# Optimization experiments

Measured on AMD Instinct MI355X. Metric: run time of the kernel, lower is better.

Reference implementation:

```python
import jax, jax.numpy as jnp
import numpy as np

B, L, D, H = 2, 2048, 1024, 16
DH = D // H
TAU = 0.1


def setup_inputs() -> dict:
    key = jax.random.key(0)
    ks = jax.random.split(key, 12)
    s = 0.02
    return {
        "q_x": jax.random.normal(ks[0], (B, L, D), jnp.float32),
        "k_x": jax.random.normal(ks[1], (B, L, D), jnp.float32),
        "v_x": jax.random.normal(ks[2], (B, L, D), jnp.float32),
        "ec": jax.random.normal(ks[3], (B, L, D), jnp.float32),
        "Wq": jax.random.normal(ks[4], (D, D), jnp.float32) * s,
        "bq": jnp.zeros((D,), jnp.float32),
        "Wk": jax.random.normal(ks[5], (D, D), jnp.float32) * s,
        "bk": jnp.zeros((D,), jnp.float32),
        "Wv": jax.random.normal(ks[6], (D, D), jnp.float32) * s,
        "bv": jnp.zeros((D,), jnp.float32),
        "Wo": jax.random.normal(ks[7], (D, D), jnp.float32) * s,
        "bo": jnp.zeros((D,), jnp.float32),
    }


def reference(q_x, k_x, v_x, ec, Wq, bq, Wk, bk, Wv, bv, Wo, bo):
    # torch nn.Linear: y = x @ W.T + b
    Q = (q_x @ Wq.T + bq).reshape(B, L, H, DH).transpose(0, 2, 1, 3)   # [B,H,L,Dh]
    K = (k_x @ Wk.T + bk).reshape(B, -1, H, DH).transpose(0, 2, 1, 3)  # [B,H,S,Dh]
    V = (v_x @ Wv.T + bv).reshape(B, -1, H, DH).transpose(0, 2, 1, 3)  # [B,H,S,Dh]
    scores = jnp.einsum("bhld,bhsd->bhls", Q, K) / jnp.sqrt(jnp.float32(DH))
    w = jnp.nan_to_num(jax.nn.softmax(scores, axis=-1), nan=0.0)       # [B,H,L,S]
    # frequency gate per key position: sigmoid((mean|ec| - tau) * 10)
    gate = jax.nn.sigmoid((jnp.abs(ec).mean(-1) - TAU) * 10.0)          # [B,S]
    w = w * gate[:, None, None, :]
    out = jnp.einsum("bhls,bhsd->bhld", w, V)                           # [B,H,L,Dh]
    out = out.transpose(0, 2, 1, 3).reshape(B, L, D)
    return out @ Wo.T + bo
```

## Files before the change

kernel.cpp:

```cpp
#include <hip/hip_runtime.h>

typedef unsigned short u16;
typedef unsigned int u32;
typedef unsigned long long u64;
typedef __attribute__((ext_vector_type(8))) short bf16x8;
typedef __attribute__((ext_vector_type(4))) float f32x4;
typedef __attribute__((ext_vector_type(2))) unsigned int u32x2;
typedef __attribute__((ext_vector_type(4))) unsigned int u32x4;

#define B_ 2
#define L_ 2048
#define D_ 1024
#define H_ 16
#define M_ 4096

__device__ __forceinline__ u16 f2bf(float f) {
  u32 x = __builtin_bit_cast(u32, f);
  return (u16)((x + 0x7fffu + ((x >> 16) & 1u)) >> 16);
}
__device__ __forceinline__ u32 cvtpk(float lo, float hi) {
  u32 r;
  asm("v_cvt_pk_bf16_f32 %0, %1, %2" : "=v"(r) : "v"(lo), "v"(hi));
  return r;
}

__device__ __forceinline__ void lane_regroup(u32& a, u32& b) {
#if __has_builtin(__builtin_amdgcn_permlane32_swap) && \
    __has_builtin(__builtin_amdgcn_permlane16_swap)
  u32x2 r = __builtin_amdgcn_permlane32_swap(a, b, false, false);
  u32x2 t = __builtin_amdgcn_permlane16_swap(r.x, r.y, false, false);
  a = t.x;
  b = t.y;
#else
  asm("v_permlane32_swap_b32 %0, %1\n\t"
      "v_permlane16_swap_b32 %0, %1"
      : "+v"(a), "+v"(b));
#endif
}

__device__ __forceinline__ void gl2lds16(void* lds, const void* g) {
  __builtin_amdgcn_global_load_lds(
      (const __attribute__((address_space(1))) u32*)g,
      (__attribute__((address_space(3))) u32*)lds, 16, 0, 0);
}

__device__ __forceinline__ void wait_vm8() {
  asm volatile("s_waitcnt vmcnt(8)" ::: "memory");
}
__device__ __forceinline__ void wait_vm6() {
  asm volatile("s_waitcnt vmcnt(6)" ::: "memory");
}
__device__ __forceinline__ void wait_vm4() {
  asm volatile("s_waitcnt vmcnt(4)" ::: "memory");
}
__device__ __forceinline__ void wait_vm0() {
  asm volatile("s_waitcnt vmcnt(0)" ::: "memory");
}
__device__ __forceinline__ void bar() {
  asm volatile("" ::: "memory");
  __builtin_amdgcn_s_barrier();
  asm volatile("" ::: "memory");
}

__global__ void cvt_all(const float* __restrict__ q, const float* __restrict__ k,
                        const float* __restrict__ v, const float* __restrict__ wq,
                        const float* __restrict__ wk, const float* __restrict__ wv,
                        const float* __restrict__ wo, const float* __restrict__ ec,
                        u16* __restrict__ Xq, u16* __restrict__ Xk, u16* __restrict__ Xv,
                        u16* __restrict__ Wqb, u16* __restrict__ Wkb,
                        u16* __restrict__ Wvb, u16* __restrict__ Wob,
                        float* __restrict__ gate) {
  if (blockIdx.x >= 16384) {
    int row = (blockIdx.x - 16384) * 4 + (threadIdx.x >> 6);
    int lane = threadIdx.x & 63;
    const float4* p = (const float4*)(ec + (size_t)row * 1024);
    float s = 0.f;
#pragma unroll
    for (int i = 0; i < 4; i++) {
      float4 vv = p[i * 64 + lane];
      s += fabsf(vv.x) + fabsf(vv.y) + fabsf(vv.z) + fabsf(vv.w);
    }
#pragma unroll
    for (int m = 1; m < 64; m <<= 1) s += __shfl_xor(s, m);
    if (lane == 0) {
      float mean = s * (1.0f / 1024.0f);
      gate[row] = 1.0f / (1.0f + __expf(-(mean - 0.1f) * 10.0f));
    }
    return;
  }
  int i = blockIdx.x * 256 + threadIdx.x;
  const float* s;
  u16* d;
  int off;
  if (i < 3145728) {
    int t = i >> 20;
    off = i & 1048575;
    s = t == 0 ? q : t == 1 ? k : v;
    d = t == 0 ? Xq : t == 1 ? Xk : Xv;
  } else {
    int j = i - 3145728;
    int t = j >> 18;
    off = j & 262143;
    s = t == 0 ? wq : t == 1 ? wk : t == 2 ? wv : wo;
    d = t == 0 ? Wqb : t == 1 ? Wkb : t == 2 ? Wvb : Wob;
  }
  float4 vv = ((const float4*)s)[off];
  ((u64*)d)[off] = (u64)cvtpk(vv.x, vv.y) | ((u64)cvtpk(vv.z, vv.w) << 32);
}

__global__ __launch_bounds__(256, 3) void gemm_qkv(
    const u16* __restrict__ Xq, const u16* __restrict__ Xk, const u16* __restrict__ Xv,
    const u16* __restrict__ Wq, const u16* __restrict__ Wk, const u16* __restrict__ Wv,
    const float* __restrict__ bq, const float* __restrict__ bk,
    const float* __restrict__ bv, const float* __restrict__ gate,
    u16* __restrict__ Qo, u16* __restrict__ Ko, u16* __restrict__ Vt) {
  __shared__ char smem[49152];
  const int which = blockIdx.x >> 9;
  const u16* A = which == 0 ? Xq : which == 1 ? Xk : Xv;
  const u16* Bw = which == 0 ? Wq : which == 1 ? Wk : Wv;
  const float* bias = which == 0 ? bq : which == 1 ? bk : bv;
  const int bi = blockIdx.x & 511;
  const int tid = threadIdx.x;
  const int tm = bi >> 3;
  const int tn = bi & 7;
  const int w = tid >> 6, lane = tid & 63;
  const int c = lane & 15, g = lane >> 4;
  const int wr = (w >> 1) << 5;
  const int wc = (w & 1) << 6;
  const int srow = tid >> 3, sch = tid & 7;

  f32x4 acc[2][4] = {};

  auto stage = [&](int buf, int t) {
    char* As = smem + buf * 24576;
    char* Bs = As + 8192;
#pragma unroll
    for (int i = 0; i < 2; i++) {
      int row = i * 32 + srow;
      int chs = (sch ^ (row & 7)) << 3;
      gl2lds16(As + i * 4096 + w * 1024, A + (size_t)(tm * 64 + row) * 1024 + t * 64 + chs);
    }
#pragma unroll
    for (int i = 0; i < 4; i++) {
      int row = i * 32 + srow;
      int chs = (sch ^ (row & 7)) << 3;
      gl2lds16(Bs + i * 4096 + w * 1024, Bw + (size_t)(tn * 128 + row) * 1024 + t * 64 + chs);
    }
  };

  stage(0, 0);
  for (int t = 0; t < 16; t++) {
    int cur = t & 1;
    if (t < 15) {
      stage(cur ^ 1, t + 1);
      wait_vm6();
    } else {
      wait_vm0();
    }
    bar();
    const char* As = smem + cur * 24576;
    const char* Bs = As + 8192;
#pragma unroll
    for (int kd = 0; kd < 2; kd++) {
      bf16x8 af[2], bfr[4];
#pragma unroll
      for (int fi = 0; fi < 2; fi++) {
        int ra = wr + fi * 16 + c;
        af[fi] = *(const bf16x8*)(As + ra * 128 + ((((kd << 2) | g) ^ (ra & 7)) << 4));
      }
#pragma unroll
      for (int fj = 0; fj < 4; fj++) {
        int rb = wc + fj * 16 + c;
        bfr[fj] = *(const bf16x8*)(Bs + rb * 128 + ((((kd << 2) | g) ^ (rb & 7)) << 4));
      }
#pragma unroll
      for (int fi = 0; fi < 2; fi++)
#pragma unroll
        for (int fj = 0; fj < 4; fj++)
          acc[fi][fj] = __builtin_amdgcn_mfma_f32_16x16x32_bf16(af[fi], bfr[fj],
                                                                acc[fi][fj], 0, 0, 0);
    }
    bar();
  }

  if (which == 2) {
    u16* T = (u16*)smem;
    __syncthreads();
#pragma unroll
    for (int fi = 0; fi < 2; fi++) {
      int lr0 = wr + fi * 16 + g * 4;
      float4 gg = *(const float4*)(gate + tm * 64 + lr0);
#pragma unroll
      for (int fj = 0; fj < 4; fj++) {
        int lc = wc + fj * 16 + c;
        float bv2 = bias[tn * 128 + lc];
        T[lc * 72 + lr0 + 0] = f2bf((acc[fi][fj][0] + bv2) * gg.x);
        T[lc * 72 + lr0 + 1] = f2bf((acc[fi][fj][1] + bv2) * gg.y);
        T[lc * 72 + lr0 + 2] = f2bf((acc[fi][fj][2] + bv2) * gg.z);
        T[lc * 72 + lr0 + 3] = f2bf((acc[fi][fj][3] + bv2) * gg.w);
      }
    }
    __syncthreads();
    const int lc = tid >> 1, hf = tid & 1;
    const int vtrow = (tm >> 5) * 1024 + tn * 128 + lc;
    const int s0 = (tm & 31) * 64 + hf * 32;
    const u16* src = T + lc * 72 + hf * 32;
    u16* dst = Vt + (size_t)vtrow * 2048 + s0;
#pragma unroll
    for (int j = 0; j < 4; j++)
      *(bf16x8*)(dst + j * 8) = *(const bf16x8*)(src + j * 8);
  } else {
    u16* Cout = which == 0 ? Qo : Ko;
    const float oscl = which == 0 ? 0.18033688011112042f : 1.0f;
    const int rowb = tm * 64 + wr + g * 4;
    const int colb = tn * 128 + wc + c;
#pragma unroll
    for (int fj = 0; fj < 4; fj++) {
      int col = colb + fj * 16;
      float bv2 = bias[col];
#pragma unroll
      for (int fi = 0; fi < 2; fi++) {
        int r0 = rowb + fi * 16;
#pragma unroll
        for (int r = 0; r < 4; r++)
          Cout[(size_t)(r0 + r) * 1024 + col] = f2bf((acc[fi][fj][r] + bv2) * oscl);
      }
    }
  }
}

__global__ __launch_bounds__(256, 2) void gemm_o(const u16* __restrict__ A,
                                                 const u16* __restrict__ Bw,
                                                 const float* __restrict__ bias,
                                                 float* __restrict__ Cout) {
  __shared__ char smem[49152];
  const int tid = threadIdx.x;
  const int tm = blockIdx.x >> 3;
  const int tn = blockIdx.x & 7;
  const int w = tid >> 6, lane = tid & 63;
  const int c = lane & 15, g = lane >> 4;
  const int wr = (w >> 1) << 5;
  const int wc = (w & 1) << 6;
  const int srow = tid >> 3, sch = tid & 7;

  f32x4 acc[2][4] = {};

  auto stage = [&](int buf, int t) {
    char* As = smem + buf * 24576;
    char* Bs = As + 8192;
#pragma unroll
    for (int i = 0; i < 2; i++) {
      int row = i * 32 + srow;
      int chs = (sch ^ (row & 7)) << 3;
      gl2lds16(As + i * 4096 + w * 1024, A + (size_t)(tm * 64 + row) * 1024 + t * 64 + chs);
    }
#pragma unroll
    for (int i = 0; i < 4; i++) {
      int row = i * 32 + srow;
      int chs = (sch ^ (row & 7)) << 3;
      gl2lds16(Bs + i * 4096 + w * 1024, Bw + (size_t)(tn * 128 + row) * 1024 + t * 64 + chs);
    }
  };

  stage(0, 0);
  for (int t = 0; t < 16; t++) {
    int cur = t & 1;
    if (t < 15) {
      stage(cur ^ 1, t + 1);
      wait_vm6();
    } else {
      wait_vm0();
    }
    bar();
    const char* As = smem + cur * 24576;
    const char* Bs = As + 8192;
#pragma unroll
    for (int kd = 0; kd < 2; kd++) {
      bf16x8 af[2], bfr[4];
#pragma unroll
      for (int fi = 0; fi < 2; fi++) {
        int ra = wr + fi * 16 + c;
        af[fi] = *(const bf16x8*)(As + ra * 128 + ((((kd << 2) | g) ^ (ra & 7)) << 4));
      }
#pragma unroll
      for (int fj = 0; fj < 4; fj++) {
        int rb = wc + fj * 16 + c;
        bfr[fj] = *(const bf16x8*)(Bs + rb * 128 + ((((kd << 2) | g) ^ (rb & 7)) << 4));
      }
#pragma unroll
      for (int fi = 0; fi < 2; fi++)
#pragma unroll
        for (int fj = 0; fj < 4; fj++)
          acc[fi][fj] = __builtin_amdgcn_mfma_f32_16x16x32_bf16(af[fi], bfr[fj],
                                                                acc[fi][fj], 0, 0, 0);
    }
    bar();
  }

  const int rowb = tm * 64 + wr + g * 4;
  const int colb = tn * 128 + wc + c;
#pragma unroll
  for (int fj = 0; fj < 4; fj++) {
    int col = colb + fj * 16;
    float bv2 = bias[col];
#pragma unroll
    for (int fi = 0; fi < 2; fi++) {
      int r0 = rowb + fi * 16;
#pragma unroll
      for (int r = 0; r < 4; r++)
        Cout[(size_t)(r0 + r) * 1024 + col] = acc[fi][fj][r] + bv2;
    }
  }
}

__global__ __launch_bounds__(256, 3) void attn_kernel(const u16* __restrict__ Qb,
                                                      const u16* __restrict__ Kb,
                                                      const u16* __restrict__ Vt,
                                                      u16* __restrict__ Ob) {
  __shared__ char asmem[49152];
  const int bi = blockIdx.x;
  const int bh = (bi & 7) | ((bi >> 7) << 3);
  const int qt = (bi >> 3) & 15;
  const int b = bh >> 4, h = bh & 15;
  const int tid = threadIdx.x, w = tid >> 6, lane = tid & 63;
  const int c = lane & 15, g = lane >> 4;
  const int qrow0 = b * L_ + qt * 128 + w * 32;

  bf16x8 qf[2][2];
#pragma unroll
  for (int fj = 0; fj < 2; fj++)
#pragma unroll
    for (int kd = 0; kd < 2; kd++)
      qf[fj][kd] = *(const bf16x8*)(Qb + (size_t)(qrow0 + fj * 16 + c) * D_ + h * 64 +
                                    kd * 32 + g * 8);

  const u32x4 onew = {0x3F803F80u, 0x3F803F80u, 0x3F803F80u, 0x3F803F80u};
  const bf16x8 one8 = __builtin_bit_cast(bf16x8, onew);

  f32x4 oacc[4][2] = {};
  f32x4 oaccD[2] = {};

  const int srow = tid >> 3, sch = tid & 7;
  const int vrow = tid >> 4, vch = tid & 15;

  auto stageK = [&](int buf, int kv) {
    char* KsB = asmem + buf * 16384;
    int sbase = kv * 128;
#pragma unroll
    for (int i = 0; i < 4; i++) {
      int kr = i * 32 + srow;
      gl2lds16(KsB + i * 4096 + w * 1024,
               Kb + (size_t)(b * L_ + sbase + kr) * D_ + h * 64 + ((sch ^ (kr & 7)) << 3));
    }
  };
  auto stageV = [&](int kv) {
    char* VsB = asmem + 32768;
    int sbase = kv * 128;
#pragma unroll
    for (int i = 0; i < 4; i++) {
      int vr = i * 16 + vrow;
      gl2lds16(VsB + i * 4096 + w * 1024,
               Vt + (size_t)(bh * 64 + vr) * 2048 + sbase + ((vch ^ (vr & 15)) << 3));
    }
  };

  stageK(0, 0);
  stageV(0);
  int buf = 0;
  for (int kv = 0; kv < 16; kv++) {
    if (kv < 15) {
      stageK(buf ^ 1, kv + 1);
      wait_vm8();
    } else {
      wait_vm4();
    }
    bar();
    const char* Ks = asmem + buf * 16384;
    const char* Vs = asmem + 32768;

    f32x4 st0[8] = {}, st1[8] = {};
    __builtin_amdgcn_s_setprio(1);
#pragma unroll
    for (int kd = 0; kd < 2; kd++) {
#pragma unroll
      for (int fi = 0; fi < 8; fi++) {
        int row = fi * 16 + c;
        bf16x8 kf = *(const bf16x8*)(Ks + row * 128 + ((((kd << 2) | g) ^ (c & 7)) << 4));
        st0[fi] = __builtin_amdgcn_mfma_f32_16x16x32_bf16(kf, qf[0][kd], st0[fi], 0, 0, 0);
        st1[fi] = __builtin_amdgcn_mfma_f32_16x16x32_bf16(kf, qf[1][kd], st1[fi], 0, 0, 0);
      }
    }
    __builtin_amdgcn_s_setprio(0);

    u32 pkA0[8], pkB0[8], pkA1[8], pkB1[8];
#pragma unroll
    for (int fi = 0; fi < 8; fi++) {
      pkA0[fi] = cvtpk(__builtin_amdgcn_exp2f(st0[fi][0]), __builtin_amdgcn_exp2f(st0[fi][1]));
      pkB0[fi] = cvtpk(__builtin_amdgcn_exp2f(st0[fi][2]), __builtin_amdgcn_exp2f(st0[fi][3]));
    }
#pragma unroll
    for (int fi = 0; fi < 8; fi++) {
      pkA1[fi] = cvtpk(__builtin_amdgcn_exp2f(st1[fi][0]), __builtin_amdgcn_exp2f(st1[fi][1]));
      pkB1[fi] = cvtpk(__builtin_amdgcn_exp2f(st1[fi][2]), __builtin_amdgcn_exp2f(st1[fi][3]));
    }

    if (kv < 15)
      wait_vm4();
    else
      wait_vm0();

    __builtin_amdgcn_s_setprio(1);
#pragma unroll
    for (int ks = 0; ks < 4; ks++) {
      u32 a0 = pkA0[2 * ks], b0 = pkA0[2 * ks + 1];
      lane_regroup(a0, b0);
      u32 a1 = pkB0[2 * ks], b1 = pkB0[2 * ks + 1];
      lane_regroup(a1, b1);
      u32x4 pw0 = {a0, a1, b0, b1};
      bf16x8 pf0 = __builtin_bit_cast(bf16x8, pw0);
      u32 e0 = pkA1[2 * ks], f0 = pkA1[2 * ks + 1];
      lane_regroup(e0, f0);
      u32 e1 = pkB1[2 * ks], f1 = pkB1[2 * ks + 1];
      lane_regroup(e1, f1);
      u32x4 pw1 = {e0, e1, f0, f1};
      bf16x8 pf1 = __builtin_bit_cast(bf16x8, pw1);
      oaccD[0] = __builtin_amdgcn_mfma_f32_16x16x32_bf16(one8, pf0, oaccD[0], 0, 0, 0);
      oaccD[1] = __builtin_amdgcn_mfma_f32_16x16x32_bf16(one8, pf1, oaccD[1], 0, 0, 0);
#pragma unroll
      for (int fd = 0; fd < 4; fd++) {
        int vr2 = fd * 16 + c;
        bf16x8 vf = *(const bf16x8*)(Vs + vr2 * 256 + ((((ks << 2) | g) ^ (vr2 & 15)) << 4));
        oacc[fd][0] = __builtin_amdgcn_mfma_f32_16x16x32_bf16(vf, pf0, oacc[fd][0], 0, 0, 0);
        oacc[fd][1] = __builtin_amdgcn_mfma_f32_16x16x32_bf16(vf, pf1, oacc[fd][1], 0, 0, 0);
      }
    }
    __builtin_amdgcn_s_setprio(0);
    bar();
    if (kv < 15) stageV(kv + 1);
    buf ^= 1;
  }

#pragma unroll
  for (int fj = 0; fj < 2; fj++) {
    float inv = 1.0f / oaccD[fj][0];
    size_t orow = (size_t)(qrow0 + fj * 16 + c) * D_ + h * 64;
#pragma unroll
    for (int fd = 0; fd < 4; fd++) {
      u64 pk = (u64)cvtpk(oacc[fd][fj][0] * inv, oacc[fd][fj][1] * inv) |
               ((u64)cvtpk(oacc[fd][fj][2] * inv, oacc[fd][fj][3] * inv) << 32);
      *(u64*)(Ob + orow + fd * 16 + g * 4) = pk;
    }
  }
}

extern "C" void kernel_launch(void* const* d_in, const int* in_sizes, int n_in,
                              void* d_out, int out_size, void* d_ws, size_t ws_size,
                              hipStream_t stream) {
  const float* q_x = (const float*)d_in[0];
  const float* k_x = (const float*)d_in[1];
  const float* v_x = (const float*)d_in[2];
  const float* ec = (const float*)d_in[3];
  const float* Wq = (const float*)d_in[4];
  const float* bq = (const float*)d_in[5];
  const float* Wk = (const float*)d_in[6];
  const float* bk = (const float*)d_in[7];
  const float* Wv = (const float*)d_in[8];
  const float* bv = (const float*)d_in[9];
  const float* Wo = (const float*)d_in[10];
  const float* bo = (const float*)d_in[11];

  char* ws = (char*)d_ws;
  const size_t MB = 1024 * 1024;
  u16* Wqb = (u16*)(ws + 0 * MB);
  u16* Wkb = (u16*)(ws + 2 * MB);
  u16* Wvb = (u16*)(ws + 4 * MB);
  u16* Wob = (u16*)(ws + 6 * MB);
  float* gatep = (float*)(ws + 8 * MB);
  u16* Xq = (u16*)(ws + 9 * MB);
  u16* Xk = (u16*)(ws + 17 * MB);
  u16* Xv = (u16*)(ws + 25 * MB);
  u16* Qb = (u16*)(ws + 33 * MB);
  u16* Kb = (u16*)(ws + 41 * MB);
  u16* Vtb = (u16*)(ws + 49 * MB);
  u16* Ab = Xk;

  cvt_all<<<17408, 256, 0, stream>>>(q_x, k_x, v_x, Wq, Wk, Wv, Wo, ec, Xq, Xk, Xv,
                                     Wqb, Wkb, Wvb, Wob, gatep);
  gemm_qkv<<<1536, 256, 0, stream>>>(Xq, Xk, Xv, Wqb, Wkb, Wvb, bq, bk, bv, gatep, Qb,
                                     Kb, Vtb);
  attn_kernel<<<512, 256, 0, stream>>>(Qb, Kb, Vtb, Ab);
  gemm_o<<<512, 256, 0, stream>>>(Ab, Wob, bo, (float*)d_out);
}
```

Baseline: 115.0 us.

## Fuse fp32-to-bf16 activation conversion into QKV GEMM A-tile loading

Removes the separate conversion pass for the three fp32 activation tensors. The QKV GEMM now loads fp32 A tiles into registers, converts them to bf16 and writes them into swizzled LDS, with the next tile's load issued before the MFMA loop. This drops a 24MB write and reread of bf16 copies but doubles the GEMM's A-side global traffic and replaces async global-to-LDS loads with register staging that raises register pressure.

```diff
diff --git a/kernel.cpp b/kernel.cpp
--- a/kernel.cpp
+++ b/kernel.cpp
@@ -56,22 +56,22 @@
 __device__ __forceinline__ void wait_vm0() {
   asm volatile("s_waitcnt vmcnt(0)" ::: "memory");
 }
+__device__ __forceinline__ void wait_lgkm0() {
+  asm volatile("s_waitcnt lgkmcnt(0)" ::: "memory");
+}
 __device__ __forceinline__ void bar() {
   asm volatile("" ::: "memory");
   __builtin_amdgcn_s_barrier();
   asm volatile("" ::: "memory");
 }
 
-__global__ void cvt_all(const float* __restrict__ q, const float* __restrict__ k,
-                        const float* __restrict__ v, const float* __restrict__ wq,
-                        const float* __restrict__ wk, const float* __restrict__ wv,
-                        const float* __restrict__ wo, const float* __restrict__ ec,
-                        u16* __restrict__ Xq, u16* __restrict__ Xk, u16* __restrict__ Xv,
-                        u16* __restrict__ Wqb, u16* __restrict__ Wkb,
-                        u16* __restrict__ Wvb, u16* __restrict__ Wob,
-                        float* __restrict__ gate) {
-  if (blockIdx.x >= 16384) {
-    int row = (blockIdx.x - 16384) * 4 + (threadIdx.x >> 6);
+__global__ void cvt_all(const float* __restrict__ wq, const float* __restrict__ wk,
+                        const float* __restrict__ wv, const float* __restrict__ wo,
+                        const float* __restrict__ ec, u16* __restrict__ Wqb,
+                        u16* __restrict__ Wkb, u16* __restrict__ Wvb,
+                        u16* __restrict__ Wob, float* __restrict__ gate) {
+  if (blockIdx.x >= 4096) {
+    int row = (blockIdx.x - 4096) * 4 + (threadIdx.x >> 6);
     int lane = threadIdx.x & 63;
     const float4* p = (const float4*)(ec + (size_t)row * 1024);
     float s = 0.f;
@@ -89,34 +89,24 @@
     return;
   }
   int i = blockIdx.x * 256 + threadIdx.x;
-  const float* s;
-  u16* d;
-  int off;
-  if (i < 3145728) {
-    int t = i >> 20;
-    off = i & 1048575;
-    s = t == 0 ? q : t == 1 ? k : v;
-    d = t == 0 ? Xq : t == 1 ? Xk : Xv;
-  } else {
-    int j = i - 3145728;
-    int t = j >> 18;
-    off = j & 262143;
-    s = t == 0 ? wq : t == 1 ? wk : t == 2 ? wv : wo;
-    d = t == 0 ? Wqb : t == 1 ? Wkb : t == 2 ? Wvb : Wob;
-  }
+  int t = i >> 18;
+  int off = i & 262143;
+  const float* s = t == 0 ? wq : t == 1 ? wk : t == 2 ? wv : wo;
+  u16* d = t == 0 ? Wqb : t == 1 ? Wkb : t == 2 ? Wvb : Wob;
   float4 vv = ((const float4*)s)[off];
   ((u64*)d)[off] = (u64)cvtpk(vv.x, vv.y) | ((u64)cvtpk(vv.z, vv.w) << 32);
 }
 
 __global__ __launch_bounds__(256, 3) void gemm_qkv(
-    const u16* __restrict__ Xq, const u16* __restrict__ Xk, const u16* __restrict__ Xv,
-    const u16* __restrict__ Wq, const u16* __restrict__ Wk, const u16* __restrict__ Wv,
+    const float* __restrict__ Xq, const float* __restrict__ Xk,
+    const float* __restrict__ Xv, const u16* __restrict__ Wq,
+    const u16* __restrict__ Wk, const u16* __restrict__ Wv,
     const float* __restrict__ bq, const float* __restrict__ bk,
     const float* __restrict__ bv, const float* __restrict__ gate,
     u16* __restrict__ Qo, u16* __restrict__ Ko, u16* __restrict__ Vt) {
   __shared__ char smem[49152];
   const int which = blockIdx.x >> 9;
-  const u16* A = which == 0 ? Xq : which == 1 ? Xk : Xv;
+  const float* A = which == 0 ? Xq : which == 1 ? Xk : Xv;
   const u16* Bw = which == 0 ? Wq : which == 1 ? Wk : Wv;
   const float* bias = which == 0 ? bq : which == 1 ? bk : bv;
   const int bi = blockIdx.x & 511;
@@ -129,17 +119,32 @@
   const int wc = (w & 1) << 6;
   const int srow = tid >> 3, sch = tid & 7;
 
+  const int arow = tid >> 2;
+  const int acs = (tid & 3) << 4;
+  const int aj0 = (tid & 3) << 1;
+
   f32x4 acc[2][4] = {};
-
-  auto stage = [&](int buf, int t) {
+  float4 ra0, ra1, ra2, ra3;
+
+  auto regloadA = [&](int t) {
+    const float4* src =
+        (const float4*)(A + (size_t)(tm * 64 + arow) * 1024 + t * 64 + acs);
+    ra0 = src[0];
+    ra1 = src[1];
+    ra2 = src[2];
+    ra3 = src[3];
+  };
+  auto writeA = [&](int buf) {
     char* As = smem + buf * 24576;
-    char* Bs = As + 8192;
-#pragma unroll
-    for (int i = 0; i < 2; i++) {
-      int row = i * 32 + srow;
-      int chs = (sch ^ (row & 7)) << 3;
-      gl2lds16(As + i * 4096 + w * 1024, A + (size_t)(tm * 64 + row) * 1024 + t * 64 + chs);
-    }
+    u32x4 w0 = {cvtpk(ra0.x, ra0.y), cvtpk(ra0.z, ra0.w), cvtpk(ra1.x, ra1.y),
+                cvtpk(ra1.z, ra1.w)};
+    u32x4 w1 = {cvtpk(ra2.x, ra2.y), cvtpk(ra2.z, ra2.w), cvtpk(ra3.x, ra3.y),
+                cvtpk(ra3.z, ra3.w)};
+    *(u32x4*)(As + arow * 128 + (((aj0 + 0) ^ (arow & 7)) << 4)) = w0;
+    *(u32x4*)(As + arow * 128 + (((aj0 + 1) ^ (arow & 7)) << 4)) = w1;
+  };
+  auto stageB = [&](int buf, int t) {
+    char* Bs = smem + buf * 24576 + 8192;
 #pragma unroll
     for (int i = 0; i < 4; i++) {
       int row = i * 32 + srow;
@@ -148,12 +153,17 @@
     }
   };
 
-  stage(0, 0);
+  regloadA(0);
+  stageB(0, 0);
+  writeA(0);
+  wait_lgkm0();
+
   for (int t = 0; t < 16; t++) {
     int cur = t & 1;
     if (t < 15) {
-      stage(cur ^ 1, t + 1);
-      wait_vm6();
+      regloadA(t + 1);
+      stageB(cur ^ 1, t + 1);
+      wait_vm8();
     } else {
       wait_vm0();
     }
@@ -179,6 +189,10 @@
         for (int fj = 0; fj < 4; fj++)
           acc[fi][fj] = __builtin_amdgcn_mfma_f32_16x16x32_bf16(af[fi], bfr[fj],
                                                                 acc[fi][fj], 0, 0, 0);
+    }
+    if (t < 15) {
+      writeA(cur ^ 1);
+      wait_lgkm0();
     }
     bar();
   }
@@ -476,18 +490,14 @@
   u16* Wvb = (u16*)(ws + 4 * MB);
   u16* Wob = (u16*)(ws + 6 * MB);
   float* gatep = (float*)(ws + 8 * MB);
-  u16* Xq = (u16*)(ws + 9 * MB);
-  u16* Xk = (u16*)(ws + 17 * MB);
-  u16* Xv = (u16*)(ws + 25 * MB);
+  u16* Ab = (u16*)(ws + 9 * MB);
   u16* Qb = (u16*)(ws + 33 * MB);
   u16* Kb = (u16*)(ws + 41 * MB);
   u16* Vtb = (u16*)(ws + 49 * MB);
-  u16* Ab = Xk;
-
-  cvt_all<<<17408, 256, 0, stream>>>(q_x, k_x, v_x, Wq, Wk, Wv, Wo, ec, Xq, Xk, Xv,
-                                     Wqb, Wkb, Wvb, Wob, gatep);
-  gemm_qkv<<<1536, 256, 0, stream>>>(Xq, Xk, Xv, Wqb, Wkb, Wvb, bq, bk, bv, gatep, Qb,
-                                     Kb, Vtb);
+
+  cvt_all<<<5120, 256, 0, stream>>>(Wq, Wk, Wv, Wo, ec, Wqb, Wkb, Wvb, Wob, gatep);
+  gemm_qkv<<<1536, 256, 0, stream>>>(q_x, k_x, v_x, Wqb, Wkb, Wvb, bq, bk, bv, gatep,
+                                     Qb, Kb, Vtb);
   attn_kernel<<<512, 256, 0, stream>>>(Qb, Kb, Vtb, Ab);
   gemm_o<<<512, 256, 0, stream>>>(Ab, Wob, bo, (float*)d_out);
 }
```

Result: slower. 129.1 us (+12.3%).
